# Performance work log

Measured on AMD Instinct MI355X. Metric: run time of the kernel, lower is better.

Reference implementation:

```python
import jax, jax.numpy as jnp
import numpy as np
from jax import lax

B = 4096
E = 8
D = 9216       # model_dim = 64*12*12
H = 128        # hidden_size_per_expert
O = 10         # output_dim


def setup_inputs() -> dict:
    key = jax.random.key(0)
    ks = jax.random.split(key, 10)
    s = lambda *sh: 1.0 / np.sqrt(np.prod(sh[1:]) if len(sh) > 1 else sh[0])
    return {
        "x": jax.random.normal(ks[0], (B, 1, 28, 28), jnp.float32),
        "conv1_w": jax.random.normal(ks[1], (32, 1, 3, 3), jnp.float32) * s(32, 1, 3, 3),
        "conv1_b": jnp.zeros((32,), jnp.float32),
        "conv2_w": jax.random.normal(ks[2], (64, 32, 3, 3), jnp.float32) * s(64, 32, 3, 3),
        "conv2_b": jnp.zeros((64,), jnp.float32),
        "gate_w": jax.random.normal(ks[3], (D, E), jnp.float32) * s(D, E),
        "w1": jax.random.normal(ks[4], (E, D, H), jnp.float32) * s(E, D, H),
        "b1": jnp.zeros((E, H), jnp.float32),
        "w2": jax.random.normal(ks[5], (E, H, O), jnp.float32) * s(E, H, O),
        "b2": jnp.zeros((E, O), jnp.float32),
    }


def _conv(x, w, b):
    y = lax.conv_general_dilated(x, w, (1, 1), "VALID",
                                 dimension_numbers=("NCHW", "OIHW", "NCHW"))
    return y + b[None, :, None, None]


def _maxpool2(x):
    return lax.reduce_window(x, -jnp.inf, lax.max,
                             (1, 1, 2, 2), (1, 1, 2, 2), "VALID")


def reference(x, conv1_w, conv1_b, conv2_w, conv2_b, gate_w, w1, b1, w2, b2):
    h = jax.nn.relu(_conv(x, conv1_w, conv1_b))            # [B,32,26,26]
    h = jax.nn.relu(_conv(h, conv2_w, conv2_b))            # [B,64,24,24]
    h = _maxpool2(h)                                       # [B,64,12,12]
    h = h.reshape(h.shape[0], -1)                          # [B,D]

    # top-1 gate: softmax over expert logits, pick argmax, scale by its prob
    logits = h @ gate_w                                    # [B,E]
    gates = jax.nn.softmax(logits, axis=-1)
    idx = jnp.argmax(logits, axis=-1)                      # [B]
    scale = jnp.take_along_axis(gates, idx[:, None], axis=1)  # [B,1]

    # expert FFN (computed densely per expert, selected per token)
    he = jax.nn.relu(jnp.einsum("bd,edh->beh", h, w1) + b1)   # [B,E,H]
    oe = jnp.einsum("beh,eho->beo", he, w2) + b2              # [B,E,O]
    out = jnp.take_along_axis(oe, idx[:, None, None], axis=1)[:, 0]  # [B,O]
    out = scale * out
    return jax.nn.log_softmax(out, axis=-1)
```

## Files before the change

kernel.cpp:

```cpp
#include <hip/hip_runtime.h>
#include <math.h>

namespace {
constexpr int kB = 4096;
constexpr int kD = 9216;
constexpr int kE = 8;
constexpr int kH = 128;
constexpr int kO = 10;
constexpr int PSTR = 32;
constexpr int KSPLIT = 8;

typedef __attribute__((ext_vector_type(8))) short short8;
typedef __attribute__((ext_vector_type(4))) float f32x4;

__device__ inline unsigned f2bf(float f) {
  unsigned u = __float_as_uint(f);
  return (u + 0x7fffu + ((u >> 16) & 1u)) >> 16;
}
__device__ inline float bf2f(unsigned b) { return __uint_as_float(b << 16); }

__global__ __launch_bounds__(256) void prep_w1(
    const float* __restrict__ w1, ushort* __restrict__ w1ph,
    ushort* __restrict__ w1pl, const float* __restrict__ c2w,
    ushort* __restrict__ Bph, ushort* __restrict__ Bpl,
    int* __restrict__ counts) {
  if (blockIdx.x == 0) {
    if (threadIdx.x < kE) counts[threadIdx.x] = 0;
    for (int i = threadIdx.x; i < 9 * 4 * 64 * 8; i += 256) {
      int j = i & 7, lane = (i >> 3) & 63, nt = (i >> 9) & 3, tap = i >> 11;
      int n = nt * 16 + (lane & 15);
      int c1 = (lane >> 4) * 8 + j;
      float v = c2w[(n * 32 + c1) * 9 + tap];
      unsigned hb = f2bf(v);
      Bph[i] = (ushort)hb;
      Bpl[i] = (ushort)f2bf(v - bf2f(hb));
    }
  }
  int t = blockIdx.x * 256 + threadIdx.x;
  int n = t & 127;
  int rem = t >> 7;
  int k8 = rem % 1152;
  int e = rem / 1152;
  const float* src = w1 + ((size_t)e * kD + (size_t)k8 * 8) * kH + n;
  short8 sh, sl;
#pragma unroll
  for (int j = 0; j < 8; ++j) {
    float v = src[(size_t)j * kH];
    unsigned hb = f2bf(v);
    sh[j] = (short)hb;
    sl[j] = (short)f2bf(v - bf2f(hb));
  }
  size_t base =
      ((((size_t)e * 288 + (k8 >> 2)) * 8 + (n >> 4)) * 64 +
       (((k8 & 3) << 4) | (n & 15))) * 8;
  *(short8*)(w1ph + base) = sh;
  *(short8*)(w1pl + base) = sl;
}

__global__ __launch_bounds__(256, 2) void conv_kernel(
    const float* __restrict__ x, const float* __restrict__ c1w,
    const float* __restrict__ c1b, const float* __restrict__ b2g,
    const ushort* __restrict__ Bph, const ushort* __restrict__ Bpl,
    float* __restrict__ h) {
  __shared__ float xs[784];
  __shared__ float w1s[288];
  __shared__ float b1s[32];
  __shared__ ushort h1h[364 * PSTR];
  __shared__ ushort h1l[364 * PSTR];
  const int b = blockIdx.x, tid = threadIdx.x;
  const int lane = tid & 63, wave = tid >> 6;

  short8 Bh[9], Bl[9];
#pragma unroll
  for (int tap = 0; tap < 9; ++tap) {
    int fi = ((tap * 4 + wave) * 64 + lane) * 8;
    Bh[tap] = *(const short8*)(Bph + fi);
    Bl[tap] = *(const short8*)(Bpl + fi);
  }
  float b2v = b2g[wave * 16 + (lane & 15)];

  const float* xb = x + (size_t)b * 784;
  for (int i = tid; i < 784; i += 256) xs[i] = xb[i];
  for (int i = tid; i < 288; i += 256) w1s[i] = c1w[i];
  if (tid < 32) b1s[tid] = c1b[tid];
  __syncthreads();

  float* hb = h + (size_t)b * kD;
  for (int pass = 0; pass < 2; ++pass) {
    for (int i = tid; i < 364 * 16; i += 256) {
      int p = i >> 4, cp = (i & 15) * 2;
      int r = p / 26, col = p - r * 26;
      const float* xr = xs + (pass * 12 + r) * 28 + col;
      const float* w0 = w1s + cp * 9;
      float v0 = b1s[cp], v1 = b1s[cp + 1];
#pragma unroll
      for (int ky = 0; ky < 3; ++ky)
#pragma unroll
        for (int kx = 0; kx < 3; ++kx) {
          float xv = xr[ky * 28 + kx];
          v0 += xv * w0[ky * 3 + kx];
          v1 += xv * w0[9 + ky * 3 + kx];
        }
      v0 = fmaxf(v0, 0.f);
      v1 = fmaxf(v1, 0.f);
      unsigned h0 = f2bf(v0), h1b = f2bf(v1);
      unsigned l0 = f2bf(v0 - bf2f(h0)), l1 = f2bf(v1 - bf2f(h1b));
      *(unsigned*)&h1h[p * PSTR + cp] = h0 | (h1b << 16);
      *(unsigned*)&h1l[p * PSTR + cp] = l0 | (l1 << 16);
    }
    __syncthreads();
    const int m = lane & 15, kg = lane >> 4;
    for (int mt = 0; mt < 18; ++mt) {
      int cell = mt * 4 + (m >> 2), sub = m & 3;
      int cy = cell / 12, cx = cell - cy * 12;
      int yy = 2 * cy + (sub >> 1), xx = 2 * cx + (sub & 1);
      const ushort* ah = h1h + (yy * 26 + xx) * PSTR + kg * 8;
      const ushort* al = h1l + (yy * 26 + xx) * PSTR + kg * 8;
      f32x4 acc = {0.f, 0.f, 0.f, 0.f};
#pragma unroll
      for (int ky = 0; ky < 3; ++ky)
#pragma unroll
        for (int kx = 0; kx < 3; ++kx) {
          const int tap = ky * 3 + kx;
          short8 Ah = *(const short8*)(ah + (ky * 26 + kx) * PSTR);
          short8 Al = *(const short8*)(al + (ky * 26 + kx) * PSTR);
          acc = __builtin_amdgcn_mfma_f32_16x16x32_bf16(Al, Bh[tap], acc, 0, 0, 0);
          acc = __builtin_amdgcn_mfma_f32_16x16x32_bf16(Ah, Bl[tap], acc, 0, 0, 0);
          acc = __builtin_amdgcn_mfma_f32_16x16x32_bf16(Ah, Bh[tap], acc, 0, 0, 0);
        }
      int cellg = mt * 4 + kg;
      int gy = cellg / 12, gx = cellg - gy * 12;
      int orow = (pass * 6 + gy) * 12 + gx;
      float p0 = fmaxf(fmaxf(acc[0], acc[1]), fmaxf(acc[2], acc[3]));
      hb[(wave * 16 + m) * 144 + orow] = fmaxf(p0 + b2v, 0.f);
    }
    __syncthreads();
  }
}

__global__ __launch_bounds__(256) void gate_kernel(
    const float* __restrict__ h, const float* __restrict__ gw,
    int* __restrict__ idx, float* __restrict__ scale,
    int* __restrict__ counts) {
  const int b = blockIdx.x * 4 + (threadIdx.x >> 6);
  const int lane = threadIdx.x & 63;
  const float* hb = h + (size_t)b * kD;
  float acc[kE] = {0, 0, 0, 0, 0, 0, 0, 0};
  for (int i = lane; i < kD; i += 64) {
    float hv = hb[i];
    const float* g = gw + (size_t)i * kE;
#pragma unroll
    for (int e = 0; e < kE; ++e) acc[e] += hv * g[e];
  }
#pragma unroll
  for (int off = 32; off > 0; off >>= 1) {
#pragma unroll
    for (int e = 0; e < kE; ++e) acc[e] += __shfl_down(acc[e], off, 64);
  }
  if (lane == 0) {
    float m = acc[0];
    int bi = 0;
#pragma unroll
    for (int e = 1; e < kE; ++e)
      if (acc[e] > m) { m = acc[e]; bi = e; }
    float s = 0.f;
#pragma unroll
    for (int e = 0; e < kE; ++e) s += expf(acc[e] - m);
    idx[b] = bi;
    scale[b] = 1.0f / s;
    atomicAdd(&counts[bi], 1);
  }
}

__global__ __launch_bounds__(256) void scan_scatter(
    const int* __restrict__ counts, const int* __restrict__ idx,
    int* __restrict__ offsets, int* __restrict__ perm) {
  __shared__ int soff[kE + 1];
  __shared__ int cur[kE];
  if (threadIdx.x == 0) {
    int o = 0;
    for (int e = 0; e < kE; ++e) {
      soff[e] = o;
      cur[e] = o;
      o += counts[e];
    }
    soff[kE] = o;
  }
  __syncthreads();
  for (int b = threadIdx.x; b < kB; b += 256) {
    int e = idx[b];
    int pos = atomicAdd(&cur[e], 1);
    perm[pos] = b;
  }
  if (threadIdx.x <= kE) offsets[threadIdx.x] = soff[threadIdx.x];
}

__global__ __launch_bounds__(256) void expert_gemm(
    const float* __restrict__ h, const ushort* __restrict__ w1ph,
    const ushort* __restrict__ w1pl, const int* __restrict__ perm,
    const int* __restrict__ offsets, float* __restrict__ preact) {
  const int e = blockIdx.x, ks = blockIdx.y;
  const int start = offsets[e] + blockIdx.z * 64;
  const int end = offsets[e + 1];
  if (start >= end) return;
  const int M = min(64, end - start);
  __shared__ ushort Afh[4096];
  __shared__ ushort Afl[4096];
  __shared__ ushort Bsh[8192];
  __shared__ ushort Bsl[8192];
  __shared__ int rows[64];
  const int tid = threadIdx.x;
  if (tid < 64) rows[tid] = perm[start + min(tid, M - 1)];
  __syncthreads();
  const int wave = tid >> 6, lane = tid & 63;
  const int m15 = lane & 15, kg4 = lane >> 4;
  const int srow = tid >> 2, spart = tid & 3;
  const int kbase = ks * (kD / KSPLIT);
  const float* hp0 = h + (size_t)rows[srow] * kD + kbase + spart * 16;
  const int skstep = spart >> 1, skg = (spart & 1) * 2;
  const int sg = srow >> 4, sm = srow & 15;
  ushort* wh0 = &Afh[((skstep * 4 + sg) * 64 + skg * 16 + sm) * 8];
  ushort* wl0 = &Afl[((skstep * 4 + sg) * 64 + skg * 16 + sm) * 8];
  f32x4 acc[8];
#pragma unroll
  for (int j = 0; j < 8; ++j) acc[j] = {0.f, 0.f, 0.f, 0.f};

  for (int bk = 0; bk < kD / KSPLIT; bk += 64) {
#pragma unroll
    for (int c = 0; c < 2; ++c) {
      float4 v0 = *(const float4*)(hp0 + bk + c * 8);
      float4 v1 = *(const float4*)(hp0 + bk + c * 8 + 4);
      short8 ph, pl;
      float f[8] = {v0.x, v0.y, v0.z, v0.w, v1.x, v1.y, v1.z, v1.w};
#pragma unroll
      for (int j = 0; j < 8; ++j) {
        unsigned hb = f2bf(f[j]);
        ph[j] = (short)hb;
        pl[j] = (short)f2bf(f[j] - bf2f(hb));
      }
      *(short8*)(wh0 + c * 128) = ph;
      *(short8*)(wl0 + c * 128) = pl;
    }
    {
      const size_t bbase =
          ((size_t)e * 288 + ((kbase + bk) >> 5)) * 4096;
#pragma unroll
      for (int q = 0; q < 4; ++q) {
        int c = tid + q * 256;
        *(short8*)&Bsh[c * 8] = *(const short8*)(w1ph + bbase + (size_t)c * 8);
        *(short8*)&Bsl[c * 8] = *(const short8*)(w1pl + bbase + (size_t)c * 8);
      }
    }
    __syncthreads();
#pragma unroll
    for (int kstep = 0; kstep < 2; ++kstep) {
      const ushort* af = &Afh[((kstep * 4 + wave) * 64 + lane) * 8];
      short8 ah = *(const short8*)af;
      short8 al = *(const short8*)(af + (Afl - Afh));
      const ushort* bph = &Bsh[kstep * 4096 + lane * 8];
      const ushort* bpl = &Bsl[kstep * 4096 + lane * 8];
#pragma unroll
      for (int nt = 0; nt < 8; ++nt) {
        short8 bh = *(const short8*)(bph + nt * 512);
        short8 bl = *(const short8*)(bpl + nt * 512);
        acc[nt] = __builtin_amdgcn_mfma_f32_16x16x32_bf16(al, bh, acc[nt], 0, 0, 0);
        acc[nt] = __builtin_amdgcn_mfma_f32_16x16x32_bf16(ah, bl, acc[nt], 0, 0, 0);
        acc[nt] = __builtin_amdgcn_mfma_f32_16x16x32_bf16(ah, bh, acc[nt], 0, 0, 0);
      }
    }
    __syncthreads();
  }
  float* pb = preact + (size_t)ks * kB * kH;
#pragma unroll
  for (int r = 0; r < 4; ++r) {
    int row = wave * 16 + kg4 * 4 + r;
    if (row < M) {
      float* pr = pb + (size_t)rows[row] * kH + m15;
#pragma unroll
      for (int nt = 0; nt < 8; ++nt) pr[nt * 16] = acc[nt][r];
    }
  }
}

__global__ __launch_bounds__(64) void expert_tail(
    const float* __restrict__ preact, const float* __restrict__ b1,
    const float* __restrict__ w2, const float* __restrict__ b2,
    const int* __restrict__ idx, const float* __restrict__ scale,
    float* __restrict__ out) {
  const int b = blockIdx.x;
  const int lane = threadIdx.x;
  const int e = idx[b];
  float pa = 0.f, pc = 0.f;
#pragma unroll
  for (int ks = 0; ks < KSPLIT; ++ks) {
    const float* ps = preact + ((size_t)ks * kB + b) * kH;
    pa += ps[lane];
    pc += ps[64 + lane];
  }
  float hea = fmaxf(pa + b1[e * kH + lane], 0.f);
  float heb = fmaxf(pc + b1[e * kH + 64 + lane], 0.f);
  const float* w2a = w2 + ((size_t)e * kH + lane) * kO;
  const float* w2b = w2a + 64 * kO;
  float part[kO];
#pragma unroll
  for (int o = 0; o < kO; ++o) part[o] = hea * w2a[o] + heb * w2b[o];
#pragma unroll
  for (int off = 32; off > 0; off >>= 1)
#pragma unroll
    for (int o = 0; o < kO; ++o) part[o] += __shfl_down(part[o], off, 64);
  if (lane == 0) {
    const float sc = scale[b];
    float v[kO], m = -1e30f;
#pragma unroll
    for (int o = 0; o < kO; ++o) {
      v[o] = (part[o] + b2[e * kO + o]) * sc;
      m = fmaxf(m, v[o]);
    }
    float s = 0.f;
#pragma unroll
    for (int o = 0; o < kO; ++o) s += expf(v[o] - m);
    const float lse = m + logf(s);
#pragma unroll
    for (int o = 0; o < kO; ++o) out[(size_t)b * kO + o] = v[o] - lse;
  }
}

}

extern "C" void kernel_launch(void* const* d_in, const int* in_sizes, int n_in,
                              void* d_out, int out_size, void* d_ws,
                              size_t ws_size, hipStream_t stream) {
  (void)in_sizes; (void)n_in; (void)out_size; (void)ws_size;
  const float* x   = (const float*)d_in[0];
  const float* c1w = (const float*)d_in[1];
  const float* c1b = (const float*)d_in[2];
  const float* c2w = (const float*)d_in[3];
  const float* c2b = (const float*)d_in[4];
  const float* gw  = (const float*)d_in[5];
  const float* w1  = (const float*)d_in[6];
  const float* b1  = (const float*)d_in[7];
  const float* w2  = (const float*)d_in[8];
  const float* b2  = (const float*)d_in[9];
  float* out = (float*)d_out;

  char* ws = (char*)d_ws;
  float* h = (float*)ws;
  size_t off = (size_t)kB * kD * sizeof(float);
  ushort* w1ph = (ushort*)(ws + off); off += (size_t)kE * kD * kH * 2;
  ushort* w1pl = (ushort*)(ws + off); off += (size_t)kE * kD * kH * 2;
  float* preact = (float*)(ws + off); off += (size_t)KSPLIT * kB * kH * 4;
  ushort* Bph = (ushort*)(ws + off);  off += 9 * 4 * 64 * 8 * 2;
  ushort* Bpl = (ushort*)(ws + off);  off += 9 * 4 * 64 * 8 * 2;
  int* idx = (int*)(ws + off);        off += (size_t)kB * 4;
  float* scale = (float*)(ws + off);  off += (size_t)kB * 4;
  int* perm = (int*)(ws + off);       off += (size_t)kB * 4;
  int* counts = (int*)(ws + off);     off += 64;
  int* offsets = (int*)(ws + off);    off += 64;

  prep_w1<<<4608, 256, 0, stream>>>(w1, w1ph, w1pl, c2w, Bph, Bpl, counts);
  conv_kernel<<<kB, 256, 0, stream>>>(x, c1w, c1b, c2b, Bph, Bpl, h);
  gate_kernel<<<kB / 4, 256, 0, stream>>>(h, gw, idx, scale, counts);
  scan_scatter<<<1, 256, 0, stream>>>(counts, idx, offsets, perm);
  dim3 eg(kE, KSPLIT, 16);
  expert_gemm<<<eg, 256, 0, stream>>>(h, w1ph, w1pl, perm, offsets, preact);
  expert_tail<<<kB, 64, 0, stream>>>(preact, b1, w2, b2, idx, scale, out);
}
```

Before: 543.0 us.

## Retile conv2 MFMA work so each wave computes 2 N-tiles by 9 M-tiles

The conv2 implicit GEMM previously had each wave own one 16-channel N tile and loop over all 18 M tiles, reloading A fragments from LDS for every wave. Now each wave owns two N tiles and half of the M tiles, processed three at a time with six independent accumulators. Each A fragment loaded from LDS is reused across two N tiles, which halves LDS reads, and the independent MFMA chains add instruction-level parallelism. In exchange the wave holds twice as many B fragments plus more accumulators, which raises VGPR pressure and may affect occupancy under launch_bounds(256,2).

```diff
diff --git a/kernel.cpp b/kernel.cpp
--- a/kernel.cpp
+++ b/kernel.cpp
@@ -69,15 +69,22 @@
   __shared__ ushort h1l[364 * PSTR];
   const int b = blockIdx.x, tid = threadIdx.x;
   const int lane = tid & 63, wave = tid >> 6;
-
-  short8 Bh[9], Bl[9];
-#pragma unroll
-  for (int tap = 0; tap < 9; ++tap) {
-    int fi = ((tap * 4 + wave) * 64 + lane) * 8;
-    Bh[tap] = *(const short8*)(Bph + fi);
-    Bl[tap] = *(const short8*)(Bpl + fi);
-  }
-  float b2v = b2g[wave * 16 + (lane & 15)];
+  const int n0 = (wave & 1) * 2;
+  const int mtb = (wave >> 1) * 9;
+  const int m = lane & 15, kg = lane >> 4;
+
+  short8 Bh[2][9], Bl[2][9];
+#pragma unroll
+  for (int nt = 0; nt < 2; ++nt)
+#pragma unroll
+    for (int tap = 0; tap < 9; ++tap) {
+      int fi = ((tap * 4 + n0 + nt) * 64 + lane) * 8;
+      Bh[nt][tap] = *(const short8*)(Bph + fi);
+      Bl[nt][tap] = *(const short8*)(Bpl + fi);
+    }
+  float b2v[2];
+  b2v[0] = b2g[n0 * 16 + m];
+  b2v[1] = b2g[(n0 + 1) * 16 + m];
 
   const float* xb = x + (size_t)b * 784;
   for (int i = tid; i < 784; i += 256) xs[i] = xb[i];
@@ -109,30 +116,54 @@
       *(unsigned*)&h1l[p * PSTR + cp] = l0 | (l1 << 16);
     }
     __syncthreads();
-    const int m = lane & 15, kg = lane >> 4;
-    for (int mt = 0; mt < 18; ++mt) {
-      int cell = mt * 4 + (m >> 2), sub = m & 3;
-      int cy = cell / 12, cx = cell - cy * 12;
-      int yy = 2 * cy + (sub >> 1), xx = 2 * cx + (sub & 1);
-      const ushort* ah = h1h + (yy * 26 + xx) * PSTR + kg * 8;
-      const ushort* al = h1l + (yy * 26 + xx) * PSTR + kg * 8;
-      f32x4 acc = {0.f, 0.f, 0.f, 0.f};
+#pragma unroll
+    for (int c = 0; c < 3; ++c) {
+      f32x4 acc[3][2];
+#pragma unroll
+      for (int i = 0; i < 3; ++i) {
+        acc[i][0] = {0.f, 0.f, 0.f, 0.f};
+        acc[i][1] = {0.f, 0.f, 0.f, 0.f};
+      }
+      int pbase[3];
+#pragma unroll
+      for (int i = 0; i < 3; ++i) {
+        int mt = mtb + c * 3 + i;
+        int cell = mt * 4 + (m >> 2), sub = m & 3;
+        int cy = cell / 12, cx = cell - cy * 12;
+        int yy = 2 * cy + (sub >> 1), xx = 2 * cx + (sub & 1);
+        pbase[i] = (yy * 26 + xx) * PSTR + kg * 8;
+      }
 #pragma unroll
       for (int ky = 0; ky < 3; ++ky)
 #pragma unroll
         for (int kx = 0; kx < 3; ++kx) {
           const int tap = ky * 3 + kx;
-          short8 Ah = *(const short8*)(ah + (ky * 26 + kx) * PSTR);
-          short8 Al = *(const short8*)(al + (ky * 26 + kx) * PSTR);
-          acc = __builtin_amdgcn_mfma_f32_16x16x32_bf16(Al, Bh[tap], acc, 0, 0, 0);
-          acc = __builtin_amdgcn_mfma_f32_16x16x32_bf16(Ah, Bl[tap], acc, 0, 0, 0);
-          acc = __builtin_amdgcn_mfma_f32_16x16x32_bf16(Ah, Bh[tap], acc, 0, 0, 0);
+          const int toff = (ky * 26 + kx) * PSTR;
+#pragma unroll
+          for (int i = 0; i < 3; ++i) {
+            short8 Ah = *(const short8*)(h1h + pbase[i] + toff);
+            short8 Al = *(const short8*)(h1l + pbase[i] + toff);
+            acc[i][0] = __builtin_amdgcn_mfma_f32_16x16x32_bf16(Al, Bh[0][tap], acc[i][0], 0, 0, 0);
+            acc[i][0] = __builtin_amdgcn_mfma_f32_16x16x32_bf16(Ah, Bl[0][tap], acc[i][0], 0, 0, 0);
+            acc[i][0] = __builtin_amdgcn_mfma_f32_16x16x32_bf16(Ah, Bh[0][tap], acc[i][0], 0, 0, 0);
+            acc[i][1] = __builtin_amdgcn_mfma_f32_16x16x32_bf16(Al, Bh[1][tap], acc[i][1], 0, 0, 0);
+            acc[i][1] = __builtin_amdgcn_mfma_f32_16x16x32_bf16(Ah, Bl[1][tap], acc[i][1], 0, 0, 0);
+            acc[i][1] = __builtin_amdgcn_mfma_f32_16x16x32_bf16(Ah, Bh[1][tap], acc[i][1], 0, 0, 0);
+          }
         }
-      int cellg = mt * 4 + kg;
-      int gy = cellg / 12, gx = cellg - gy * 12;
-      int orow = (pass * 6 + gy) * 12 + gx;
-      float p0 = fmaxf(fmaxf(acc[0], acc[1]), fmaxf(acc[2], acc[3]));
-      hb[(wave * 16 + m) * 144 + orow] = fmaxf(p0 + b2v, 0.f);
+#pragma unroll
+      for (int i = 0; i < 3; ++i) {
+        int mt = mtb + c * 3 + i;
+        int cellg = mt * 4 + kg;
+        int gy = cellg / 12, gx = cellg - gy * 12;
+        int orow = (pass * 6 + gy) * 12 + gx;
+#pragma unroll
+        for (int nt = 0; nt < 2; ++nt) {
+          float p0 = fmaxf(fmaxf(acc[i][nt][0], acc[i][nt][1]),
+                           fmaxf(acc[i][nt][2], acc[i][nt][3]));
+          hb[((n0 + nt) * 16 + m) * 144 + orow] = fmaxf(p0 + b2v[nt], 0.f);
+        }
+      }
     }
     __syncthreads();
   }
```

New measurement: 565.2 us. 4.1% more time.
